# Kernel optimization log

Hardware: AMD Instinct MI355X
Metric: run time of the kernel (lower is better)

The kernel has to match this reference:

```python
import jax, jax.numpy as jnp
import numpy as np

DIMS = 4

def mlp(x, W1, b1, W2, b2, W3, b3, Wo, bo):
    # x: (4,) -> scalar log(g_rr)
    h = jnp.tanh(x @ W1 + b1)
    h = jnp.tanh(h @ W2 + b2)
    h = jnp.tanh(h @ W3 + b3)
    return (h @ Wo + bo)[0]

def metric(x, params):
    # build_g: spherical metric with learned g_rr = exp(net(x))
    g_rr = jnp.exp(mlp(x, *params))
    r, th = x[1], x[2]
    diag = jnp.stack([-jnp.ones(()), g_rr, r ** 2, (r * jnp.sin(th)) ** 2])
    return jnp.diag(diag)  # (4,4)

def christoffel(x, params):
    g = metric(x, params)
    dg = jax.jacfwd(lambda xx: metric(xx, params))(x)  # dg[i,j,k] = d g_ij / d x^k
    g_inv = jnp.linalg.inv(g)
    # Gamma^a_bc = 0.5 g^{ad} (d_c g_db + d_b g_dc - d_d g_bc)
    sym = dg + jnp.transpose(dg, (0, 2, 1)) - jnp.transpose(dg, (2, 0, 1))
    gamma = 0.5 * jnp.einsum('ad,dbc->abc', g_inv, sym)
    return gamma, g_inv

def einstein_per_sample(x, params):
    gamma, g_inv = christoffel(x, params)
    # D[a,i,j,k] = d_k Gamma^a_ij (second nested forward-mode jacobian)
    D = jax.jacfwd(lambda xx: christoffel(xx, params)[0])(x)
    # R^a_bcd = d_c Gamma^a_db - d_d Gamma^a_cb + G^a_ce G^e_db - G^a_de G^e_cb
    riemann = (jnp.einsum('adbc->abcd', D) - jnp.einsum('acbd->abcd', D)
               + jnp.einsum('ace,edb->abcd', gamma, gamma)
               - jnp.einsum('ade,ecb->abcd', gamma, gamma))
    ricci = jnp.einsum('abad->bd', riemann)
    ricci_scalar = jnp.einsum('bd,bd->', g_inv, ricci)
    ricci_up = jnp.einsum('ac,bd,cd->ab', g_inv, g_inv, ricci)
    return ricci_up - 0.5 * g_inv * ricci_scalar  # contravariant Einstein tensor


def setup_inputs() -> dict:
    key = jax.random.key(0)
    ks = jax.random.split(key, 5)
    B, H = 8192, 256
    # coords in a well-conditioned region (avoid r ~ 0 which makes g singular)
    coords = jax.random.uniform(ks[0], (B, DIMS), dtype=jnp.float32) * 0.9 + 0.1
    def w(k, shape):
        fan_in = shape[0]
        return jax.random.normal(k, shape, dtype=jnp.float32) / np.sqrt(fan_in)
    return {
        'coords': coords,
        'W1': w(ks[1], (DIMS, H)), 'b1': jnp.zeros((H,), jnp.float32),
        'W2': w(ks[2], (H, H)),   'b2': jnp.zeros((H,), jnp.float32),
        'W3': w(ks[3], (H, H)),   'b3': jnp.zeros((H,), jnp.float32),
        'Wo': w(ks[4], (H, 1)),   'bo': jnp.zeros((1,), jnp.float32),
    }


def reference(coords, W1, b1, W2, b2, W3, b3, Wo, bo):
    params = (W1, b1, W2, b2, W3, b3, Wo, bo)
    # Batched Einstein tensor G^{ab}(x) for every sample: (B, 4, 4)
    return jax.vmap(lambda x: einstein_per_sample(x, params))(coords)
```

## Files before the change

kernel.cpp:

```cpp
#include <hip/hip_runtime.h>
#include <math.h>

typedef _Float16 half8 __attribute__((ext_vector_type(8)));
typedef float floatx4 __attribute__((ext_vector_type(4)));

#define HDIM 256
#define NC 15
#define NCP 16
#define SPB 8
#define MR 128
#define NWAVE 4
#define NT 4


__device__ __forceinline__ float ftanh(float x) {
    float e = __expf(2.f * x);
    return fmaf(-2.f, __builtin_amdgcn_rcpf(e + 1.f), 1.f);
}

__device__ __forceinline__ void einstein_tail(
    float f, const float* Gf, const float* Hs, float r, float th,
    float* __restrict__ outp)
{
    float Hf[4][4];
    {
        int qq = 0;
#pragma unroll
        for (int k = 0; k < 4; ++k)
#pragma unroll
            for (int l = k; l < 4; ++l) { Hf[k][l] = Hs[qq]; Hf[l][k] = Hs[qq]; ++qq; }
    }
    float sn = sinf(th), cs = cosf(th);
    float E  = expf(f);

    float gd[4] = {-1.f, E, r * r, r * r * sn * sn};
    float gi[4];
#pragma unroll
    for (int a = 0; a < 4; ++a) gi[a] = 1.f / gd[a];

    float dgv[4][4];
    float ddg[4][4][4];
#pragma unroll
    for (int a = 0; a < 4; ++a)
#pragma unroll
        for (int k = 0; k < 4; ++k) {
            dgv[a][k] = 0.f;
#pragma unroll
            for (int l = 0; l < 4; ++l) ddg[a][k][l] = 0.f;
        }
#pragma unroll
    for (int k = 0; k < 4; ++k) dgv[1][k] = E * Gf[k];
    dgv[2][1] = 2.f * r;
    dgv[3][1] = 2.f * r * sn * sn;
    dgv[3][2] = 2.f * r * r * sn * cs;
#pragma unroll
    for (int k = 0; k < 4; ++k)
#pragma unroll
        for (int l = 0; l < 4; ++l)
            ddg[1][k][l] = E * fmaf(Gf[k], Gf[l], Hf[k][l]);
    ddg[2][1][1] = 2.f;
    ddg[3][1][1] = 2.f * sn * sn;
    ddg[3][1][2] = 4.f * r * sn * cs;
    ddg[3][2][1] = 4.f * r * sn * cs;
    ddg[3][2][2] = 2.f * r * r * (cs * cs - sn * sn);

    auto SYMF = [&](int a, int i, int jx) -> float {
        float sy = 0.f;
        if (a == i)  sy += dgv[a][jx];
        if (a == jx) sy += dgv[a][i];
        if (i == jx) sy -= dgv[i][a];
        return sy;
    };
    auto DF = [&](int a, int i, int jx, int k) -> float {
        float ds = 0.f;
        if (a == i)  ds += ddg[a][jx][k];
        if (a == jx) ds += ddg[a][i][k];
        if (i == jx) ds -= ddg[i][a][k];
        return 0.5f * (gi[a] * ds - gi[a] * gi[a] * dgv[a][k] * SYMF(a, i, jx));
    };

    float Gm[4][4][4];
#pragma unroll
    for (int a = 0; a < 4; ++a)
#pragma unroll
        for (int i = 0; i < 4; ++i)
#pragma unroll
            for (int jx = 0; jx < 4; ++jx)
                Gm[a][i][jx] = 0.5f * gi[a] * SYMF(a, i, jx);

    float ric[4][4];
#pragma unroll
    for (int b = 0; b < 4; ++b)
#pragma unroll
        for (int d = 0; d < 4; ++d) {
            float sum = 0.f;
#pragma unroll
            for (int a = 0; a < 4; ++a) {
                sum += DF(a, d, b, a) - DF(a, a, b, d);
#pragma unroll
                for (int e = 0; e < 4; ++e)
                    sum += Gm[a][a][e] * Gm[e][d][b] - Gm[a][d][e] * Gm[e][a][b];
            }
            ric[b][d] = sum;
        }

    float Rs = 0.f;
#pragma unroll
    for (int b = 0; b < 4; ++b) Rs += gi[b] * ric[b][b];

#pragma unroll
    for (int a = 0; a < 4; ++a)
#pragma unroll
        for (int b = 0; b < 4; ++b) {
            float v = gi[a] * gi[b] * ric[a][b];
            if (a == b) v -= 0.5f * gi[a] * Rs;
            outp[a * 4 + b] = v;
        }
}

__global__ __launch_bounds__(64) void einstein_k(
    const float* __restrict__ coords, const float* __restrict__ bo,
    float* io, int B)
{
    const int s = blockIdx.x * 64 + threadIdx.x;
    if (s >= B) return;
    float4 f0 = *(const float4*)&io[s * 16 + 0];
    float4 f1 = *(const float4*)&io[s * 16 + 4];
    float4 f2 = *(const float4*)&io[s * 16 + 8];
    float4 f3 = *(const float4*)&io[s * 16 + 12];
    float f = f0.x + bo[0];
    float Gf[4] = {f0.y, f0.z, f0.w, f1.x};
    float Hs[10] = {f1.y, f1.z, f1.w, f2.x, f2.y, f2.z, f2.w, f3.x, f3.y, f3.z};
    float r  = coords[s * 4 + 1];
    float th = coords[s * 4 + 2];
    float res[16];
    einstein_tail(f, Gf, Hs, r, th, res);
#pragma unroll
    for (int e = 0; e < 4; ++e)
        *(float4*)&io[s * 16 + e * 4] =
            make_float4(res[e*4+0], res[e*4+1], res[e*4+2], res[e*4+3]);
}

__global__ __launch_bounds__(256) void pack_wt(
    const float* __restrict__ W2, const float* __restrict__ W3,
    _Float16* __restrict__ Wt)
{
    __shared__ float t[64][65];
    const int m    = blockIdx.x >> 4;
    const float* W = m ? W3 : W2;
    const int tile = blockIdx.x & 15;
    const int k0 = (tile >> 2) * 64, j0 = (tile & 3) * 64;
    const int tx = threadIdx.x & 63, ty = threadIdx.x >> 6;
#pragma unroll
    for (int i = 0; i < 16; ++i) {
        int k = ty + i * 4;
        t[k][tx] = W[(k0 + k) * HDIM + j0 + tx];
    }
    __syncthreads();
#pragma unroll
    for (int i = 0; i < 16; ++i) {
        int jj = ty + i * 4;
        Wt[(size_t)m * HDIM * HDIM + (j0 + jj) * HDIM + k0 + tx] =
            (_Float16)t[tx][jj];
    }
}

template <bool TW>
__global__ __launch_bounds__(512, 2) void mlp_fused(
    const float* __restrict__ coords,
    const float* __restrict__ W1, const float* __restrict__ b1,
    const float* __restrict__ W2, const float* __restrict__ b2,
    const float* __restrict__ W3, const float* __restrict__ b3,
    const float* __restrict__ Wo,
    const _Float16* __restrict__ Wt,
    float* __restrict__ out, int B)
{
    __shared__ __align__(16) _Float16 st[2][MR * HDIM];

    const int tid  = threadIdx.x;
    const int team = tid >> 8;
    const int ttid = tid & 255;
    const int w    = ttid >> 6;
    const int lane = tid & 63;
    const int col  = lane & 15;
    const int q    = lane >> 4;
    const int s0   = blockIdx.x * (2 * SPB);
    const int sb   = s0 + team * SPB;

    _Float16* __restrict__ stT = st[team];

    floatx4 acc[8][NT];

    auto f4get = [](const float4& v, int i) -> float {
        switch (i & 3) { case 0: return v.x; case 1: return v.y;
                         case 2: return v.z; default: return v.w; }
    };

    auto produce1 = [&]() {
        const int sl = ttid & 7;
        const int tc = ttid >> 3;
        int ss = sb + sl; if (ss >= B) ss = B - 1;
        const float x0 = coords[ss * 4 + 0];
        const float x1 = coords[ss * 4 + 1];
        const float x2 = coords[ss * 4 + 2];
        const float x3 = coords[ss * 4 + 3];
        const int jg = tc * 8;
        float4 wa[4][2];
#pragma unroll
        for (int k = 0; k < 4; ++k) {
            wa[k][0] = *(const float4*)&W1[k * HDIM + jg];
            wa[k][1] = *(const float4*)&W1[k * HDIM + jg + 4];
        }
        float4 bb0 = *(const float4*)&b1[jg];
        float4 bb1 = *(const float4*)&b1[jg + 4];
        half8 ch[NCP];
#pragma unroll
        for (int jj = 0; jj < 8; ++jj) ch[15][jj] = (_Float16)0.f;
#pragma unroll
        for (int jj = 0; jj < 8; ++jj) {
            const int h = jj >> 2;
            float w0 = f4get(wa[0][h], jj), w1 = f4get(wa[1][h], jj);
            float w2v = f4get(wa[2][h], jj), w3v = f4get(wa[3][h], jj);
            float a = f4get(h ? bb1 : bb0, jj);
            a = fmaf(x0, w0, a); a = fmaf(x1, w1, a);
            a = fmaf(x2, w2v, a); a = fmaf(x3, w3v, a);
            float v = ftanh(a), tp = 1.f - v * v, m2 = -2.f * v * tp;
            float g[4] = {w0, w1, w2v, w3v};
            ch[0][jj] = (_Float16)v;
#pragma unroll
            for (int k = 0; k < 4; ++k) ch[1 + k][jj] = (_Float16)(tp * g[k]);
            int idx = 5;
#pragma unroll
            for (int aa = 0; aa < 4; ++aa)
#pragma unroll
                for (int bb2 = aa; bb2 < 4; ++bb2) {
                    ch[idx][jj] = (_Float16)(m2 * g[aa] * g[bb2]); ++idx;
                }
        }
#pragma unroll
        for (int c = 0; c < NCP; ++c) {
            const int m = 16 * (c >> 1) + 4 * (sl >> 1) + 2 * (sl & 1) + (c & 1);
            const int addr = m * HDIM + (((tc ^ m) & 31) << 3);
            *(half8*)&stT[addr] = ch[c];
        }
    };

    auto init_acc = [&](const float* __restrict__ b) {
#pragma unroll
        for (int nt = 0; nt < NT; ++nt) {
            float bj = b[w * 64 + nt * 16 + col];
#pragma unroll
            for (int mt = 0; mt < 8; ++mt)
#pragma unroll
                for (int r = 0; r < 4; ++r) acc[mt][nt][r] = 0.f;
            acc[0][nt][0] = bj;
            acc[0][nt][2] = bj;
        }
    };

    auto gemm_full = [&](const float* __restrict__ W, int layer) {
        half8 bf[2][NT];
#pragma unroll
        for (int nt = 0; nt < NT; ++nt) {
            const int j = w * 64 + nt * 16 + col;
            if constexpr (TW) {
                bf[0][nt] = *(const half8*)&Wt[((size_t)layer * HDIM + j) * HDIM + q * 8];
            } else {
#pragma unroll
                for (int i = 0; i < 8; ++i)
                    bf[0][nt][i] = (_Float16)W[(q * 8 + i) * HDIM + j];
            }
        }
#pragma unroll
        for (int ks = 0; ks < 8; ++ks) {
            const int cur = ks & 1, nxt = cur ^ 1;
            if (ks < 7) {
                const int kg2 = (ks + 1) * 32 + q * 8;
#pragma unroll
                for (int nt = 0; nt < NT; ++nt) {
                    const int j = w * 64 + nt * 16 + col;
                    if constexpr (TW) {
                        bf[nxt][nt] = *(const half8*)&Wt[((size_t)layer * HDIM + j) * HDIM + kg2];
                    } else {
#pragma unroll
                        for (int i = 0; i < 8; ++i)
                            bf[nxt][nt][i] = (_Float16)W[(kg2 + i) * HDIM + j];
                    }
                }
            }
            const int lc = ks * 4 + q;
            half8 af[8];
#pragma unroll
            for (int mt = 0; mt < 8; ++mt) {
                const int m = 16 * mt + col;
                af[mt] = *(const half8*)&stT[m * HDIM + (((lc ^ m) & 31) << 3)];
            }
#pragma unroll
            for (int mt = 0; mt < 8; ++mt)
#pragma unroll
                for (int nt = 0; nt < NT; ++nt)
                    acc[mt][nt] = __builtin_amdgcn_mfma_f32_16x16x32_f16(
                        af[mt], bf[cur][nt], acc[mt][nt], 0, 0, 0);
        }
    };

    auto transform_store = [&]() {
#pragma unroll
        for (int nt = 0; nt < NT; ++nt) {
            const int j = w * 64 + nt * 16 + col;
            const int jc = j >> 3, jb = j & 7;
#pragma unroll
            for (int sv = 0; sv < 2; ++sv) {
                float pre[NCP];
#pragma unroll
                for (int c = 0; c < NCP; ++c)
                    pre[c] = acc[c >> 1][nt][sv * 2 + (c & 1)];
                float v = ftanh(pre[0]), tp = 1.f - v * v, m2 = -2.f * v * tp;
                float g[4] = {pre[1], pre[2], pre[3], pre[4]};
                float ns[NCP];
                ns[0] = v;
#pragma unroll
                for (int k = 0; k < 4; ++k) ns[1 + k] = tp * g[k];
                int idx = 5;
#pragma unroll
                for (int aa = 0; aa < 4; ++aa)
#pragma unroll
                    for (int bb2 = aa; bb2 < 4; ++bb2) {
                        ns[idx] = fmaf(tp, pre[idx], m2 * g[aa] * g[bb2]); ++idx;
                    }
                ns[15] = 0.f;
#pragma unroll
                for (int c = 0; c < NCP; ++c) {
                    const int m = 16 * (c >> 1) + 4 * q + 2 * sv + (c & 1);
                    stT[m * HDIM + (((jc ^ m) & 31) << 3) + jb] = (_Float16)ns[c];
                }
            }
        }
    };

    auto epilogue_part = [&]() {
        float* part = (float*)stT;
        float wo[NT];
#pragma unroll
        for (int nt = 0; nt < NT; ++nt) wo[nt] = Wo[w * 64 + nt * 16 + col];

        float on2[2][NC];
#pragma unroll
        for (int sv = 0; sv < 2; ++sv)
#pragma unroll
            for (int c = 0; c < NC; ++c) on2[sv][c] = 0.f;
#pragma unroll
        for (int nt = 0; nt < NT; ++nt)
#pragma unroll
            for (int sv = 0; sv < 2; ++sv) {
                float pre[NCP];
#pragma unroll
                for (int c = 0; c < NCP; ++c)
                    pre[c] = acc[c >> 1][nt][sv * 2 + (c & 1)];
                float v = ftanh(pre[0]), tp = 1.f - v * v, m2 = -2.f * v * tp;
                float g[4] = {pre[1], pre[2], pre[3], pre[4]};
                on2[sv][0] = fmaf(wo[nt], v, on2[sv][0]);
#pragma unroll
                for (int k = 0; k < 4; ++k)
                    on2[sv][1 + k] = fmaf(wo[nt], tp * g[k], on2[sv][1 + k]);
                int idx = 5;
#pragma unroll
                for (int aa = 0; aa < 4; ++aa)
#pragma unroll
                    for (int bb2 = aa; bb2 < 4; ++bb2) {
                        on2[sv][idx] = fmaf(wo[nt],
                            fmaf(tp, pre[idx], m2 * g[aa] * g[bb2]), on2[sv][idx]);
                        ++idx;
                    }
            }
#pragma unroll
        for (int mask = 1; mask < 16; mask <<= 1)
#pragma unroll
            for (int sv = 0; sv < 2; ++sv)
#pragma unroll
                for (int c = 0; c < NC; ++c)
                    on2[sv][c] += __shfl_xor(on2[sv][c], mask, 64);
        if (col == 0) {
#pragma unroll
            for (int sv = 0; sv < 2; ++sv)
#pragma unroll
                for (int c = 0; c < NC; ++c)
                    part[(w * SPB + 2 * q + sv) * NC + c] = on2[sv][c];
        }
    };

    auto final_reduce = [&]() {
        float* part = (float*)stT;
        if (ttid < SPB * NC) {
            const int sl = ttid / NC, c = ttid % NC;
            float v = 0.f;
#pragma unroll
            for (int ww = 0; ww < NWAVE; ++ww)
                v += part[(ww * SPB + sl) * NC + c];
            int s = sb + sl;
            if (s < B) out[s * 16 + c] = v;
        }
    };

    if (team == 0) produce1();
    __syncthreads();
    if (team == 0) { init_acc(b2); gemm_full(W2, 0); }
    else produce1();
    __syncthreads();
    if (team == 0) transform_store();
    else { init_acc(b2); gemm_full(W2, 0); }
    __syncthreads();
    if (team == 0) { init_acc(b3); gemm_full(W3, 1); }
    else transform_store();
    __syncthreads();
    if (team == 0) epilogue_part();
    else { init_acc(b3); gemm_full(W3, 1); }
    __syncthreads();
    if (team == 0) final_reduce();
    else epilogue_part();
    __syncthreads();
    if (team == 1) final_reduce();
}

extern "C" void kernel_launch(void* const* d_in, const int* in_sizes, int n_in,
                              void* d_out, int out_size, void* d_ws, size_t ws_size,
                              hipStream_t stream) {
    const float* coords = (const float*)d_in[0];
    const float* W1 = (const float*)d_in[1];
    const float* b1 = (const float*)d_in[2];
    const float* W2 = (const float*)d_in[3];
    const float* b2 = (const float*)d_in[4];
    const float* W3 = (const float*)d_in[5];
    const float* b3 = (const float*)d_in[6];
    const float* Wo = (const float*)d_in[7];
    const float* bo = (const float*)d_in[8];
    float* out = (float*)d_out;
    const int B = in_sizes[0] / 4;
    const int nblocks = (B + 2 * SPB - 1) / (2 * SPB);

    const size_t wt_bytes = (size_t)2 * HDIM * HDIM * sizeof(_Float16);
    if (ws_size >= wt_bytes) {
        _Float16* Wt = (_Float16*)d_ws;
        pack_wt<<<32, 256, 0, stream>>>(W2, W3, Wt);
        mlp_fused<true><<<nblocks, 512, 0, stream>>>(
            coords, W1, b1, W2, b2, W3, b3, Wo, Wt, out, B);
    } else {
        mlp_fused<false><<<nblocks, 512, 0, stream>>>(
            coords, W1, b1, W2, b2, W3, b3, Wo, nullptr, out, B);
    }
    einstein_k<<<(B + 63) / 64, 64, 0, stream>>>(coords, bo, out, B);
}
```

Measured before the change: 119.8 us.

## Process two sample groups per team to extend the ping-pong pipeline

Each block now handles two groups of 8 samples per team instead of one. The two-team alternating schedule is extended so the second group's layer-1 production overlaps the other team's GEMM, and pipeline fill and drain are spread over more work. Partial sums move from the reused tile buffer to a dedicated shared array so the epilogue of one group does not collide with the next group's staging. The grid shrinks by half, which can reduce parallelism across CUs, and the extra shared memory may lower occupancy.

```diff
diff --git a/kernel.cpp b/kernel.cpp
--- a/kernel.cpp
+++ b/kernel.cpp
@@ -8,6 +8,7 @@
 #define NC 15
 #define NCP 16
 #define SPB 8
+#define GPT 2
 #define MR 128
 #define NWAVE 4
 #define NT 4
@@ -176,6 +177,7 @@
     float* __restrict__ out, int B)
 {
     __shared__ __align__(16) _Float16 st[2][MR * HDIM];
+    __shared__ float part[2][GPT][NWAVE][SPB][NCP];
 
     const int tid  = threadIdx.x;
     const int team = tid >> 8;
@@ -184,8 +186,7 @@
     const int lane = tid & 63;
     const int col  = lane & 15;
     const int q    = lane >> 4;
-    const int s0   = blockIdx.x * (2 * SPB);
-    const int sb   = s0 + team * SPB;
+    const int s0   = blockIdx.x * (2 * GPT * SPB);
 
     _Float16* __restrict__ stT = st[team];
 
@@ -196,10 +197,12 @@
                          case 2: return v.z; default: return v.w; }
     };
 
-    auto produce1 = [&]() {
+    auto sbase = [&](int g) { return s0 + (team * GPT + g) * SPB; };
+
+    auto produce1 = [&](int g) {
         const int sl = ttid & 7;
         const int tc = ttid >> 3;
-        int ss = sb + sl; if (ss >= B) ss = B - 1;
+        int ss = sbase(g) + sl; if (ss >= B) ss = B - 1;
         const float x0 = coords[ss * 4 + 0];
         const float x1 = coords[ss * 4 + 1];
         const float x2 = coords[ss * 4 + 2];
@@ -225,16 +228,16 @@
             a = fmaf(x0, w0, a); a = fmaf(x1, w1, a);
             a = fmaf(x2, w2v, a); a = fmaf(x3, w3v, a);
             float v = ftanh(a), tp = 1.f - v * v, m2 = -2.f * v * tp;
-            float g[4] = {w0, w1, w2v, w3v};
+            float g4[4] = {w0, w1, w2v, w3v};
             ch[0][jj] = (_Float16)v;
 #pragma unroll
-            for (int k = 0; k < 4; ++k) ch[1 + k][jj] = (_Float16)(tp * g[k]);
+            for (int k = 0; k < 4; ++k) ch[1 + k][jj] = (_Float16)(tp * g4[k]);
             int idx = 5;
 #pragma unroll
             for (int aa = 0; aa < 4; ++aa)
 #pragma unroll
                 for (int bb2 = aa; bb2 < 4; ++bb2) {
-                    ch[idx][jj] = (_Float16)(m2 * g[aa] * g[bb2]); ++idx;
+                    ch[idx][jj] = (_Float16)(m2 * g4[aa] * g4[bb2]); ++idx;
                 }
         }
 #pragma unroll
@@ -316,17 +319,17 @@
                 for (int c = 0; c < NCP; ++c)
                     pre[c] = acc[c >> 1][nt][sv * 2 + (c & 1)];
                 float v = ftanh(pre[0]), tp = 1.f - v * v, m2 = -2.f * v * tp;
-                float g[4] = {pre[1], pre[2], pre[3], pre[4]};
+                float g4[4] = {pre[1], pre[2], pre[3], pre[4]};
                 float ns[NCP];
                 ns[0] = v;
 #pragma unroll
-                for (int k = 0; k < 4; ++k) ns[1 + k] = tp * g[k];
+                for (int k = 0; k < 4; ++k) ns[1 + k] = tp * g4[k];
                 int idx = 5;
 #pragma unroll
                 for (int aa = 0; aa < 4; ++aa)
 #pragma unroll
                     for (int bb2 = aa; bb2 < 4; ++bb2) {
-                        ns[idx] = fmaf(tp, pre[idx], m2 * g[aa] * g[bb2]); ++idx;
+                        ns[idx] = fmaf(tp, pre[idx], m2 * g4[aa] * g4[bb2]); ++idx;
                     }
                 ns[15] = 0.f;
 #pragma unroll
@@ -338,8 +341,7 @@
         }
     };
 
-    auto epilogue_part = [&]() {
-        float* part = (float*)stT;
+    auto epilogue_part = [&](int g) {
         float wo[NT];
 #pragma unroll
         for (int nt = 0; nt < NT; ++nt) wo[nt] = Wo[w * 64 + nt * 16 + col];
@@ -358,18 +360,18 @@
                 for (int c = 0; c < NCP; ++c)
                     pre[c] = acc[c >> 1][nt][sv * 2 + (c & 1)];
                 float v = ftanh(pre[0]), tp = 1.f - v * v, m2 = -2.f * v * tp;
-                float g[4] = {pre[1], pre[2], pre[3], pre[4]};
+                float g4[4] = {pre[1], pre[2], pre[3], pre[4]};
                 on2[sv][0] = fmaf(wo[nt], v, on2[sv][0]);
 #pragma unroll
                 for (int k = 0; k < 4; ++k)
-                    on2[sv][1 + k] = fmaf(wo[nt], tp * g[k], on2[sv][1 + k]);
+                    on2[sv][1 + k] = fmaf(wo[nt], tp * g4[k], on2[sv][1 + k]);
                 int idx = 5;
 #pragma unroll
                 for (int aa = 0; aa < 4; ++aa)
 #pragma unroll
                     for (int bb2 = aa; bb2 < 4; ++bb2) {
                         on2[sv][idx] = fmaf(wo[nt],
-                            fmaf(tp, pre[idx], m2 * g[aa] * g[bb2]), on2[sv][idx]);
+                            fmaf(tp, pre[idx], m2 * g4[aa] * g4[bb2]), on2[sv][idx]);
                         ++idx;
                     }
             }
@@ -385,27 +387,29 @@
             for (int sv = 0; sv < 2; ++sv)
 #pragma unroll
                 for (int c = 0; c < NC; ++c)
-                    part[(w * SPB + 2 * q + sv) * NC + c] = on2[sv][c];
+                    part[team][g][w][2 * q + sv][c] = on2[sv][c];
         }
     };
 
     auto final_reduce = [&]() {
-        float* part = (float*)stT;
         if (ttid < SPB * NC) {
             const int sl = ttid / NC, c = ttid % NC;
-            float v = 0.f;
-#pragma unroll
-            for (int ww = 0; ww < NWAVE; ++ww)
-                v += part[(ww * SPB + sl) * NC + c];
-            int s = sb + sl;
-            if (s < B) out[s * 16 + c] = v;
-        }
-    };
-
-    if (team == 0) produce1();
+#pragma unroll
+            for (int g = 0; g < GPT; ++g) {
+                float v = 0.f;
+#pragma unroll
+                for (int ww = 0; ww < NWAVE; ++ww)
+                    v += part[team][g][ww][sl][c];
+                int s = sbase(g) + sl;
+                if (s < B) out[s * 16 + c] = v;
+            }
+        }
+    };
+
+    if (team == 0) produce1(0);
     __syncthreads();
     if (team == 0) { init_acc(b2); gemm_full(W2, 0); }
-    else produce1();
+    else produce1(0);
     __syncthreads();
     if (team == 0) transform_store();
     else { init_acc(b2); gemm_full(W2, 0); }
@@ -413,11 +417,23 @@
     if (team == 0) { init_acc(b3); gemm_full(W3, 1); }
     else transform_store();
     __syncthreads();
-    if (team == 0) epilogue_part();
+    if (team == 0) { epilogue_part(0); produce1(1); }
     else { init_acc(b3); gemm_full(W3, 1); }
     __syncthreads();
+    if (team == 0) { init_acc(b2); gemm_full(W2, 0); }
+    else { epilogue_part(0); produce1(1); }
+    __syncthreads();
+    if (team == 0) transform_store();
+    else { init_acc(b2); gemm_full(W2, 0); }
+    __syncthreads();
+    if (team == 0) { init_acc(b3); gemm_full(W3, 1); }
+    else transform_store();
+    __syncthreads();
+    if (team == 0) epilogue_part(1);
+    else { init_acc(b3); gemm_full(W3, 1); }
+    __syncthreads();
     if (team == 0) final_reduce();
-    else epilogue_part();
+    else epilogue_part(1);
     __syncthreads();
     if (team == 1) final_reduce();
 }
@@ -436,7 +452,8 @@
     const float* bo = (const float*)d_in[8];
     float* out = (float*)d_out;
     const int B = in_sizes[0] / 4;
-    const int nblocks = (B + 2 * SPB - 1) / (2 * SPB);
+    const int spb_blk = 2 * GPT * SPB;
+    const int nblocks = (B + spb_blk - 1) / spb_blk;
 
     const size_t wt_bytes = (size_t)2 * HDIM * HDIM * sizeof(_Float16);
     if (ws_size >= wt_bytes) {
```

New measurement: 118.1 us. About the same (-1.4%).
